# Kernel tuning notes

Hardware: AMD Instinct MI355X
Metric: run time of the kernel (lower is better)

## Reference

```python
import jax, jax.numpy as jnp
import numpy as np

B, S, T = 32, 512, 128   # batch, source chars, target (protoform) chars
V, L = 128, 5            # char vocab len(C2I), number of languages
E, H, F = 512, 1024, 2048  # embedding_dim, model_size, feedforward_dim
START_CHAR, SEP_LANG = 1, L - 1


def setup_inputs() -> dict:
    key = jax.random.key(0)
    ks = jax.random.split(key, 32)
    f32 = jnp.float32

    def n(k, shape, fan_in):
        return jax.random.normal(k, shape, dtype=f32) * (1.0 / np.sqrt(fan_in))

    inp = {
        "src_chars": jax.random.randint(ks[0], (B, S), 0, V),
        "src_langs": jax.random.randint(ks[1], (B, S), 0, L),
        "tgt_chars": jax.random.randint(ks[2], (B, T), 0, V),
        # embedding feature extractor
        "char_emb": jax.random.normal(ks[3], (V, E), dtype=f32) * 0.02,
        "lang_emb": jax.random.normal(ks[4], (L, E), dtype=f32) * 0.02,
        "fc_W": n(ks[5], (E, 2 * E), 2 * E),
        "fc_b": jnp.zeros((E,), f32),
        # encoder GRU (PyTorch gate layout r,z,n)
        "enc_Wi": n(ks[6], (3 * H, E), E),
        "enc_Wh": n(ks[7], (3 * H, H), H),
        "enc_bi": jnp.zeros((3 * H,), f32),
        "enc_bh": jnp.zeros((3 * H,), f32),
        # decoder GRU, input = [E ; H]
        "dec_Wi": n(ks[8], (3 * H, E + H), E + H),
        "dec_Wh": n(ks[9], (3 * H, H), H),
        "dec_bi": jnp.zeros((3 * H,), f32),
        "dec_bh": jnp.zeros((3 * H,), f32),
        # attention
        "Wq": n(ks[10], (H, H), H),
        "Wk": n(ks[11], (H, H), H),
        "Wcs": n(ks[12], (H, E), E),
        # MLP H -> 2F -> F -> V
        "W1": n(ks[13], (2 * F, H), H),
        "b1": jnp.zeros((2 * F,), f32),
        "W2": n(ks[14], (F, 2 * F), 2 * F),
        "b2": jnp.zeros((F,), f32),
        "W3": n(ks[15], (V, F), F),
    }
    return inp


def _gru_step(h, x, Wi, Wh, bi, bh):
    gi = x @ Wi.T + bi            # [B, 3H]
    gh = h @ Wh.T + bh            # [B, 3H]
    ir, iz, inn = jnp.split(gi, 3, axis=-1)
    hr, hz, hn = jnp.split(gh, 3, axis=-1)
    r = jax.nn.sigmoid(ir + hr)
    z = jax.nn.sigmoid(iz + hz)
    n = jnp.tanh(inn + r * hn)
    return (1.0 - z) * n + z * h


def _mlp(x, W1, b1, W2, b2, W3):
    h = jax.nn.relu(x @ W1.T + b1)
    h = jax.nn.relu(h @ W2.T + b2)
    return h @ W3.T               # [B, V]


def reference(src_chars, src_langs, tgt_chars,
              char_emb, lang_emb, fc_W, fc_b,
              enc_Wi, enc_Wh, enc_bi, enc_bh,
              dec_Wi, dec_Wh, dec_bi, dec_bh,
              Wq, Wk, Wcs,
              W1, b1, W2, b2, W3):
    # --- feature extraction: concat(char_emb, lang_emb) -> Linear(2E -> E) ---
    def embed(c_idx, l_idx):
        ce = char_emb[c_idx]                       # [..., E]
        le = lang_emb[l_idx]                       # [..., E]
        return jnp.concatenate([ce, le], -1) @ fc_W.T + fc_b

    encoded = embed(src_chars, src_langs)          # [B, S, E]

    # --- encoder GRU over source chars ---
    def enc_step(h, x_t):
        h = _gru_step(h, x_t, enc_Wi, enc_Wh, enc_bi, enc_bh)
        return h, h

    h0 = jnp.zeros((encoded.shape[0], enc_Wh.shape[1]), encoded.dtype)
    _, enc_states = jax.lax.scan(enc_step, h0, jnp.swapaxes(encoded, 0, 1))
    enc_states = jnp.swapaxes(enc_states, 0, 1)    # [B, S, H]

    # precompute attention values: W_c_s(encoded) + W_key(keys)  [B, S, H]
    att_vals = encoded @ Wcs.T + enc_states @ Wk.T

    # --- initial decoder step: <s> embedding + last encoder state ---
    start_emb = embed(jnp.full((encoded.shape[0],), START_CHAR),
                      jnp.full((encoded.shape[0],), SEP_LANG))  # [B, E]
    context0 = enc_states[:, -1]                   # [B, H]
    d0 = jnp.zeros_like(context0)
    dec_h = _gru_step(d0, jnp.concatenate([start_emb, context0], -1),
                      dec_Wi, dec_Wh, dec_bi, dec_bh)

    tgt_emb = embed(tgt_chars, jnp.full_like(tgt_chars, SEP_LANG))  # [B, T, E]

    # --- decode T steps with teacher forcing ---
    def dec_step(carry, x_t):
        h, ctx = carry
        scores_t = _mlp(h + ctx, W1, b1, W2, b2, W3)           # [B, V]
        q = h @ Wq.T                                           # [B, H]
        att = jnp.einsum('bsh,bh->bs', enc_states, q)
        w = jax.nn.softmax(att, axis=-1)
        ctx_new = jnp.einsum('bs,bsh->bh', w, att_vals)        # [B, H]
        h_new = _gru_step(h, jnp.concatenate([x_t, ctx_new], -1),
                          dec_Wi, dec_Wh, dec_bi, dec_bh)
        return (h_new, ctx_new), scores_t

    (_, _), scores = jax.lax.scan(dec_step, (dec_h, context0),
                                  jnp.swapaxes(tgt_emb, 0, 1))
    return jnp.swapaxes(scores, 0, 1)              # [B, T, V]
```

## Files before the change

### kernel.cpp

```cpp
#include <hip/hip_runtime.h>
#include <math.h>


#define Bb 32
#define Ss 512
#define Tt 128
#define Vv 128
#define Hh 1024
#define H3 3072
#define APAD 40

typedef __attribute__((ext_vector_type(8))) short bf16x8;
typedef __attribute__((ext_vector_type(4))) float f32x4;

__device__ inline f32x4 mfma_bf16(bf16x8 a, bf16x8 b, f32x4 c) {
  return __builtin_amdgcn_mfma_f32_16x16x32_bf16(a, b, c, 0, 0, 0);
}
__device__ inline unsigned short f2bf(float f) {
  unsigned u = __builtin_bit_cast(unsigned, f);
  unsigned r = (u + 0x7fffu + ((u >> 16) & 1u)) >> 16;
  return (unsigned short)r;
}
__device__ inline float lof(unsigned u) { return __builtin_bit_cast(float, u << 16); }
__device__ inline float hif(unsigned u) { return __builtin_bit_cast(float, u & 0xffff0000u); }
__device__ inline float bf2f(unsigned short h) {
  return __builtin_bit_cast(float, ((unsigned)h) << 16);
}

#define O_ESBF   0UL
#define O_ESQ    33554432UL
#define O_AVBF   67108864UL
#define O_HCBF   100663296UL
#define O_WHE    109051904UL
#define O_WHD    115343360UL
#define O_WIC    121634816UL
#define O_WKB    127926272UL
#define O_WQT    130023424UL
#define O_W1B    132120576UL
#define O_W2B    140509184UL
#define O_W3B    157286400UL
#define O_XCAT   157810688UL
#define O_EMBFC  160432128UL
#define O_GITAB  161742848UL
#define O_AVTAB  169607168UL
#define O_DGIXT  172228608UL
#define O_GH     173801472UL
#define O_GI     174194688UL
#define O_H      174587904UL
#define O_HBF    174718976UL
#define O_CTX    174784512UL
#define O_CTXBF  174915584UL
#define O_ATTL   174981120UL

__global__ void k_xcat(const float* __restrict__ ce, const float* __restrict__ le,
                       float* __restrict__ xcat) {
  int row = blockIdx.x;
  int l = row >> 7, c = row & 127;
  int i = threadIdx.x * 4;
  float4 v;
  if (i < 512) v = *(const float4*)(ce + c * 512 + i);
  else         v = *(const float4*)(le + l * 512 + (i - 512));
  *(float4*)(xcat + (size_t)row * 1024 + i) = v;
}

__global__ void k_cvt(const float* __restrict__ src, int ld, int lc,
                      unsigned short* __restrict__ dst) {
  size_t i = ((size_t)blockIdx.x * 256 + threadIdx.x) * 8;
  size_t r = i >> lc;
  int c = (int)(i & ((1u << lc) - 1));
  const float* s = src + r * (size_t)ld + c;
  float4 v0 = *(const float4*)s;
  float4 v1 = *(const float4*)(s + 4);
  union { unsigned short us[8]; uint4 u; } o;
  o.us[0] = f2bf(v0.x); o.us[1] = f2bf(v0.y); o.us[2] = f2bf(v0.z); o.us[3] = f2bf(v0.w);
  o.us[4] = f2bf(v1.x); o.us[5] = f2bf(v1.y); o.us[6] = f2bf(v1.z); o.us[7] = f2bf(v1.w);
  *(uint4*)(dst + i) = o.u;
}

__global__ void k_transcvt(const float* __restrict__ in, unsigned short* __restrict__ out) {
  __shared__ float t[32][33];
  int c0 = blockIdx.x * 32, r0 = blockIdx.y * 32;
  int tx = threadIdx.x, ty = threadIdx.y;
  for (int i = ty; i < 32; i += 8)
    t[i][tx] = in[(size_t)(r0 + i) * 1024 + c0 + tx];
  __syncthreads();
  for (int i = ty; i < 32; i += 8)
    out[(size_t)(c0 + i) * 1024 + r0 + tx] = f2bf(t[tx][i]);
}

template <bool BIAS>
__global__ __launch_bounds__(256) void k_gemm(
    const float* __restrict__ A, int lda, const float* __restrict__ W, int ldw,
    const float* __restrict__ bias, float* __restrict__ C, int ldc, int K) {
  __shared__ float As[8][128];
  __shared__ float Ws[8][128];
  int tid = threadIdx.x;
  int n0 = blockIdx.x * 128, m0 = blockIdx.y * 128;
  int tx = tid & 15, ty = tid >> 4;
  int lrow = tid >> 1, lseg = (tid & 1) * 4;
  const float* Ap = A + (size_t)(m0 + lrow) * lda + lseg;
  const float* Wp = W + (size_t)(n0 + lrow) * ldw + lseg;
  float acc[8][8];
#pragma unroll
  for (int i = 0; i < 8; ++i)
#pragma unroll
    for (int j = 0; j < 8; ++j) acc[i][j] = 0.f;
  for (int kt = 0; kt < K; kt += 8) {
    float4 av = *(const float4*)(Ap + kt);
    float4 wv = *(const float4*)(Wp + kt);
    __syncthreads();
    As[lseg + 0][lrow] = av.x; As[lseg + 1][lrow] = av.y;
    As[lseg + 2][lrow] = av.z; As[lseg + 3][lrow] = av.w;
    Ws[lseg + 0][lrow] = wv.x; Ws[lseg + 1][lrow] = wv.y;
    Ws[lseg + 2][lrow] = wv.z; Ws[lseg + 3][lrow] = wv.w;
    __syncthreads();
#pragma unroll
    for (int kk = 0; kk < 8; ++kk) {
      float a[8], b[8];
      *(float4*)(a + 0) = *(const float4*)(&As[kk][ty * 8 + 0]);
      *(float4*)(a + 4) = *(const float4*)(&As[kk][ty * 8 + 4]);
      *(float4*)(b + 0) = *(const float4*)(&Ws[kk][tx * 8 + 0]);
      *(float4*)(b + 4) = *(const float4*)(&Ws[kk][tx * 8 + 4]);
#pragma unroll
      for (int i = 0; i < 8; ++i)
#pragma unroll
        for (int j = 0; j < 8; ++j) acc[i][j] = fmaf(a[i], b[j], acc[i][j]);
    }
  }
#pragma unroll
  for (int i = 0; i < 8; ++i) {
    int r = m0 + ty * 8 + i;
#pragma unroll
    for (int j = 0; j < 8; ++j) {
      int c = n0 + tx * 8 + j;
      float v = acc[i][j];
      if (BIAS) v += bias[c];
      C[(size_t)r * ldc + c] = v;
    }
  }
}

template <int EPI, bool RELU, bool BIAS>
__global__ __launch_bounds__(256) void k_bgemm(
    const unsigned short* __restrict__ A, int lda,
    const unsigned short* __restrict__ W, int ldw,
    const float* __restrict__ bias, void* __restrict__ Cout, int ldc, int K,
    const float* __restrict__ avtab, const int* __restrict__ gl,
    const int* __restrict__ gc) {
  __shared__ unsigned short As[128 * APAD];
  __shared__ unsigned short Bs[128 * APAD];
  int tid = threadIdx.x;
  int n0 = blockIdx.x * 128, m0 = blockIdx.y * 128;
  int w = tid >> 6, l = tid & 63;
  int mw = (w & 1) * 64, nw = (w >> 1) * 64;
  int lrow = tid >> 1, lk = (tid & 1) * 16;
  const unsigned short* Ap = A + (size_t)(m0 + lrow) * lda + lk;
  const unsigned short* Wp = W + (size_t)(n0 + lrow) * ldw + lk;
  int fr = l & 15, fk = (l >> 4) * 8;
  f32x4 acc[4][4];
#pragma unroll
  for (int i = 0; i < 4; ++i)
#pragma unroll
    for (int j = 0; j < 4; ++j) acc[i][j] = (f32x4){0.f, 0.f, 0.f, 0.f};
  for (int kt = 0; kt < K; kt += 32) {
    uint4 a0 = *(const uint4*)(Ap + kt);
    uint4 a1 = *(const uint4*)(Ap + kt + 8);
    uint4 b0 = *(const uint4*)(Wp + kt);
    uint4 b1 = *(const uint4*)(Wp + kt + 8);
    __syncthreads();
    *(uint4*)&As[lrow * APAD + lk] = a0;
    *(uint4*)&As[lrow * APAD + lk + 8] = a1;
    *(uint4*)&Bs[lrow * APAD + lk] = b0;
    *(uint4*)&Bs[lrow * APAD + lk + 8] = b1;
    __syncthreads();
    bf16x8 af[4], bfg[4];
#pragma unroll
    for (int i = 0; i < 4; ++i) af[i] = *(const bf16x8*)&As[(mw + i * 16 + fr) * APAD + fk];
#pragma unroll
    for (int j = 0; j < 4; ++j) bfg[j] = *(const bf16x8*)&Bs[(nw + j * 16 + fr) * APAD + fk];
#pragma unroll
    for (int i = 0; i < 4; ++i)
#pragma unroll
      for (int j = 0; j < 4; ++j) acc[i][j] = mfma_bf16(af[i], bfg[j], acc[i][j]);
  }
#pragma unroll
  for (int i = 0; i < 4; ++i)
#pragma unroll
    for (int j = 0; j < 4; ++j) {
      int col = n0 + nw + j * 16 + fr;
#pragma unroll
      for (int r = 0; r < 4; ++r) {
        int row = m0 + mw + i * 16 + (l >> 4) * 4 + r;
        float v = acc[i][j][r];
        if (BIAS) v += bias[col];
        if (RELU) v = fmaxf(v, 0.f);
        if (EPI == 0) {
          ((unsigned short*)Cout)[(size_t)row * ldc + col] = f2bf(v);
        } else if (EPI == 1) {
          int cl = gl[row] * 128 + gc[row];
          ((unsigned short*)Cout)[(size_t)row * ldc + col] =
              f2bf(v + avtab[(size_t)cl * 1024 + col]);
        } else {
          int tt = row >> 5, bb = row & 31;
          ((float*)Cout)[(size_t)bb * (Tt * Vv) + tt * Vv + col] = v;
        }
      }
    }
}

__global__ __launch_bounds__(256) void k_rec(
    const unsigned short* __restrict__ A, const unsigned short* __restrict__ W,
    float* __restrict__ C, int N, int nrec,
    const unsigned short* __restrict__ esq, const float* __restrict__ h,
    const float* __restrict__ ctx, float* __restrict__ attL,
    unsigned short* __restrict__ hc) {
  __shared__ unsigned short As[32 * 1024];
  int tid = threadIdx.x;
  int id = blockIdx.x;
  if (id < nrec) {
    {
      const uint4* src = (const uint4*)A;
      uint4* dst = (uint4*)As;
#pragma unroll
      for (int i = 0; i < 16; ++i) {
        int c = i * 256 + tid;
        int m = c >> 7, kc = c & 127;
        dst[m * 128 + (kc ^ (m & 7))] = src[c];
      }
    }
    __syncthreads();
    int w = tid >> 6, l = tid & 63;
    int nb = id * 64 + w * 16;
    int fr = l & 15, fk8 = (l >> 4);
    const unsigned short* Wp = W + (size_t)(nb + fr) * 1024 + fk8 * 8;
    const bf16x8* Asv = (const bf16x8*)As;
    f32x4 acc0 = (f32x4){0.f, 0.f, 0.f, 0.f}, acc1 = acc0;
#pragma unroll 8
    for (int kt = 0; kt < 1024; kt += 32) {
      int kc8 = (kt >> 3) + fk8;
      bf16x8 bw = *(const bf16x8*)(Wp + kt);
      bf16x8 a0 = Asv[fr * 128 + (kc8 ^ (fr & 7))];
      bf16x8 a1 = Asv[(fr + 16) * 128 + (kc8 ^ (fr & 7))];
      acc0 = mfma_bf16(a0, bw, acc0);
      acc1 = mfma_bf16(a1, bw, acc1);
    }
    int col = nb + fr;
    int rb = (l >> 4) * 4;
#pragma unroll
    for (int r = 0; r < 4; ++r) {
      C[(size_t)(rb + r) * N + col] = acc0[r];
      C[(size_t)(rb + r + 16) * N + col] = acc1[r];
    }
  } else {
    float* hs = (float*)As;
    int a = id - nrec, b = a >> 3, sc = a & 7;
    for (int i = tid; i < 1024; i += 256) hs[i] = h[b * 1024 + i];
    __syncthreads();
    if (sc < 4) {
      int j = sc * 256 + tid;
      hc[b * 1024 + j] = f2bf(hs[j] + ctx[b * 1024 + j]);
    }
    int sg = tid >> 2, li = tid & 3;
    int s = sc * 64 + sg;
    const unsigned short* ep = esq + (size_t)(b * 512 + s) * 1024;
    float acc = 0.f;
#pragma unroll 4
    for (int i = 0; i < 32; ++i) {
      int k = (i * 4 + li) * 8;
      uint4 e = *(const uint4*)(ep + k);
      float4 h0 = *(const float4*)&hs[k];
      float4 h1 = *(const float4*)&hs[k + 4];
      acc += lof(e.x) * h0.x + hif(e.x) * h0.y + lof(e.y) * h0.z + hif(e.y) * h0.w +
             lof(e.z) * h1.x + hif(e.z) * h1.y + lof(e.w) * h1.z + hif(e.w) * h1.w;
    }
    acc += __shfl_xor(acc, 1);
    acc += __shfl_xor(acc, 2);
    if (li == 0) attL[b * 512 + s] = acc;
  }
}

__global__ void k_gates_enc(const float* __restrict__ gh, const float* __restrict__ gitab,
                            const int* __restrict__ sc, const int* __restrict__ sl,
                            const float* __restrict__ bh, float* __restrict__ h,
                            unsigned short* __restrict__ hbf, unsigned short* __restrict__ esb,
                            int s, int first) {
  int idx = blockIdx.x * 256 + threadIdx.x;
  int b = idx >> 10, j = idx & 1023;
  float ghr = bh[j], ghz = bh[1024 + j], ghn = bh[2048 + j];
  if (!first) {
    const float* g = gh + b * H3 + j;
    ghr += g[0]; ghz += g[1024]; ghn += g[2048];
  }
  int cl = sl[b * Ss + s] * 128 + sc[b * Ss + s];
  const float* gi = gitab + (size_t)cl * H3 + j;
  float r = 1.f / (1.f + expf(-(gi[0] + ghr)));
  float z = 1.f / (1.f + expf(-(gi[1024] + ghz)));
  float n = tanhf(gi[2048] + r * ghn);
  float hold = first ? 0.f : h[idx];
  float hn = (1.f - z) * n + z * hold;
  h[idx] = hn;
  unsigned short hb = f2bf(hn);
  hbf[idx] = hb;
  esb[(size_t)(b * Ss + s) * Hh + j] = hb;
}

__global__ void k_gates_dec(const float* __restrict__ gi, const float* __restrict__ gh,
                            const float* __restrict__ dgixt, const int* __restrict__ tgt,
                            const float* __restrict__ bh, float* __restrict__ h,
                            unsigned short* __restrict__ hbf, int t, int hzero, int usestart) {
  int idx = blockIdx.x * 256 + threadIdx.x;
  int b = idx >> 10, j = idx & 1023;
  const float* gp = gi + b * H3 + j;
  float gir = gp[0], giz = gp[1024], gin = gp[2048];
  float ghr = bh[j], ghz = bh[1024 + j], ghn = bh[2048 + j];
  if (!hzero) {
    const float* g = gh + b * H3 + j;
    ghr += g[0]; ghz += g[1024]; ghn += g[2048];
  }
  int c = usestart ? 1 : tgt[b * Tt + t];
  const float* gx = dgixt + (size_t)c * H3 + j;
  gir += gx[0]; giz += gx[1024]; gin += gx[2048];
  float r = 1.f / (1.f + expf(-(gir + ghr)));
  float z = 1.f / (1.f + expf(-(giz + ghz)));
  float n = tanhf(gin + r * ghn);
  float hold = hzero ? 0.f : h[idx];
  float hn = (1.f - z) * n + z * hold;
  h[idx] = hn;
  hbf[idx] = f2bf(hn);
}

__global__ void k_ctxinit(const float* __restrict__ h, float* __restrict__ ctx,
                          unsigned short* __restrict__ ctxbf) {
  int idx = blockIdx.x * 256 + threadIdx.x;
  float v = h[idx];
  ctx[idx] = v;
  ctxbf[idx] = f2bf(v);
}

__global__ __launch_bounds__(256) void k_ctxsm(const float* __restrict__ attL,
                                               const unsigned short* __restrict__ av,
                                               float* __restrict__ ctx,
                                               unsigned short* __restrict__ ctxbf) {
  int jt = blockIdx.x, b = blockIdx.y;
  __shared__ float w[512];
  __shared__ float wm[4];
  __shared__ float wsm[4];
  __shared__ float red2[128];
  int tid = threadIdx.x;
  float a0 = attL[b * Ss + tid * 2];
  float a1 = attL[b * Ss + tid * 2 + 1];
  float m = fmaxf(a0, a1);
  for (int d = 1; d < 64; d <<= 1) m = fmaxf(m, __shfl_xor(m, d));
  if ((tid & 63) == 0) wm[tid >> 6] = m;
  __syncthreads();
  m = fmaxf(fmaxf(wm[0], wm[1]), fmaxf(wm[2], wm[3]));
  float e0 = expf(a0 - m), e1 = expf(a1 - m);
  w[tid * 2] = e0;
  w[tid * 2 + 1] = e1;
  float ssum = e0 + e1;
  for (int d = 1; d < 64; d <<= 1) ssum += __shfl_xor(ssum, d);
  if ((tid & 63) == 0) wsm[tid >> 6] = ssum;
  __syncthreads();
  float scale = 1.f / (wsm[0] + wsm[1] + wsm[2] + wsm[3]);
  int j = jt * 128 + (tid & 127);
  int sh = tid >> 7;
  const unsigned short* avp = av + (size_t)(b * Ss + sh * 256) * Hh + j;
  float acc = 0.f;
#pragma unroll 16
  for (int s = 0; s < 256; ++s) acc += w[sh * 256 + s] * bf2f(avp[(size_t)s * Hh]);
  if (sh == 1) red2[tid & 127] = acc;
  __syncthreads();
  if (sh == 0) {
    float v = (acc + red2[tid & 127]) * scale;
    ctx[b * Hh + j] = v;
    ctxbf[b * Hh + j] = f2bf(v);
  }
}

extern "C" void kernel_launch(void* const* d_in, const int* in_sizes, int n_in,
                              void* d_out, int out_size, void* d_ws, size_t ws_size,
                              hipStream_t stream) {
  (void)in_sizes; (void)n_in; (void)out_size; (void)ws_size;
  const int*   src_chars = (const int*)d_in[0];
  const int*   src_langs = (const int*)d_in[1];
  const int*   tgt_chars = (const int*)d_in[2];
  const float* char_emb  = (const float*)d_in[3];
  const float* lang_emb  = (const float*)d_in[4];
  const float* fc_W  = (const float*)d_in[5];
  const float* fc_b  = (const float*)d_in[6];
  const float* enc_Wi = (const float*)d_in[7];
  const float* enc_Wh = (const float*)d_in[8];
  const float* enc_bi = (const float*)d_in[9];
  const float* enc_bh = (const float*)d_in[10];
  const float* dec_Wi = (const float*)d_in[11];
  const float* dec_Wh = (const float*)d_in[12];
  const float* dec_bi = (const float*)d_in[13];
  const float* dec_bh = (const float*)d_in[14];
  const float* Wq  = (const float*)d_in[15];
  const float* Wk  = (const float*)d_in[16];
  const float* Wcs = (const float*)d_in[17];
  const float* W1 = (const float*)d_in[18];
  const float* b1 = (const float*)d_in[19];
  const float* W2 = (const float*)d_in[20];
  const float* b2 = (const float*)d_in[21];
  const float* W3 = (const float*)d_in[22];
  float* out = (float*)d_out;

  char* ws = (char*)d_ws;
  unsigned short* esbf  = (unsigned short*)(ws + O_ESBF);
  unsigned short* esq   = (unsigned short*)(ws + O_ESQ);
  unsigned short* avbf  = (unsigned short*)(ws + O_AVBF);
  unsigned short* hcbf  = (unsigned short*)(ws + O_HCBF);
  unsigned short* WheB  = (unsigned short*)(ws + O_WHE);
  unsigned short* WhdB  = (unsigned short*)(ws + O_WHD);
  unsigned short* WicB  = (unsigned short*)(ws + O_WIC);
  unsigned short* WkB   = (unsigned short*)(ws + O_WKB);
  unsigned short* WqTB  = (unsigned short*)(ws + O_WQT);
  unsigned short* W1B   = (unsigned short*)(ws + O_W1B);
  unsigned short* W2B   = (unsigned short*)(ws + O_W2B);
  unsigned short* W3B   = (unsigned short*)(ws + O_W3B);
  float* xcat   = (float*)(ws + O_XCAT);
  float* embfc  = (float*)(ws + O_EMBFC);
  float* gitab  = (float*)(ws + O_GITAB);
  float* avtab  = (float*)(ws + O_AVTAB);
  float* dgixt  = (float*)(ws + O_DGIXT);
  float* ghbuf  = (float*)(ws + O_GH);
  float* gibuf  = (float*)(ws + O_GI);
  float* h      = (float*)(ws + O_H);
  unsigned short* hbf   = (unsigned short*)(ws + O_HBF);
  float* ctx    = (float*)(ws + O_CTX);
  unsigned short* ctxbf = (unsigned short*)(ws + O_CTXBF);
  float* attL   = (float*)(ws + O_ATTL);
  unsigned short* G1 = esq;
  unsigned short* G2 = avbf;

  dim3 blk(256);

  k_xcat<<<640, blk, 0, stream>>>(char_emb, lang_emb, xcat);
  k_gemm<true><<<dim3(4, 5), blk, 0, stream>>>(xcat, 1024, fc_W, 1024, fc_b, embfc, 512, 1024);
  k_gemm<true><<<dim3(24, 5), blk, 0, stream>>>(embfc, 512, enc_Wi, 512, enc_bi, gitab, H3, 512);
  k_gemm<false><<<dim3(8, 5), blk, 0, stream>>>(embfc, 512, Wcs, 512, nullptr, avtab, Hh, 512);
  k_gemm<true><<<dim3(24, 1), blk, 0, stream>>>(embfc + 512 * 512, 512, dec_Wi, 1536, dec_bi,
                                                dgixt, H3, 512);
  k_cvt<<<1536, blk, 0, stream>>>(enc_Wh, 1024, 10, WheB);
  k_cvt<<<1536, blk, 0, stream>>>(dec_Wh, 1024, 10, WhdB);
  k_cvt<<<1536, blk, 0, stream>>>(dec_Wi + 512, 1536, 10, WicB);
  k_cvt<<<512,  blk, 0, stream>>>(Wk, 1024, 10, WkB);
  k_cvt<<<2048, blk, 0, stream>>>(W1, 1024, 10, W1B);
  k_cvt<<<4096, blk, 0, stream>>>(W2, 4096, 12, W2B);
  k_cvt<<<128,  blk, 0, stream>>>(W3, 2048, 11, W3B);
  k_transcvt<<<dim3(32, 32), dim3(32, 8), 0, stream>>>(Wq, WqTB);

  for (int s = 0; s < Ss; ++s) {
    if (s > 0)
      k_rec<<<48, blk, 0, stream>>>(hbf, WheB, ghbuf, H3, 48,
                                    nullptr, nullptr, nullptr, nullptr, nullptr);
    k_gates_enc<<<128, blk, 0, stream>>>(ghbuf, gitab, src_chars, src_langs, enc_bh,
                                         h, hbf, esbf, s, s == 0 ? 1 : 0);
  }

  k_bgemm<0, false, false><<<dim3(8, 128), blk, 0, stream>>>(
      esbf, 1024, WqTB, 1024, nullptr, esq, 1024, 1024, nullptr, nullptr, nullptr);
  k_bgemm<1, false, false><<<dim3(8, 128), blk, 0, stream>>>(
      esbf, 1024, WkB, 1024, nullptr, avbf, 1024, 1024, avtab, src_langs, src_chars);

  k_ctxinit<<<128, blk, 0, stream>>>(h, ctx, ctxbf);
  k_rec<<<48, blk, 0, stream>>>(ctxbf, WicB, gibuf, H3, 48,
                                nullptr, nullptr, nullptr, nullptr, nullptr);
  k_gates_dec<<<128, blk, 0, stream>>>(gibuf, ghbuf, dgixt, tgt_chars, dec_bh,
                                       h, hbf, 0, 1, 1);

  for (int t = 0; t < Tt; ++t) {
    k_rec<<<304, blk, 0, stream>>>(hbf, WhdB, ghbuf, H3, 48,
                                   esq, h, ctx, attL, hcbf + (size_t)t * Bb * Hh);
    if (t == Tt - 1) break;
    k_ctxsm<<<dim3(8, 32), blk, 0, stream>>>(attL, avbf, ctx, ctxbf);
    k_rec<<<48, blk, 0, stream>>>(ctxbf, WicB, gibuf, H3, 48,
                                  nullptr, nullptr, nullptr, nullptr, nullptr);
    k_gates_dec<<<128, blk, 0, stream>>>(gibuf, ghbuf, dgixt, tgt_chars, dec_bh,
                                         h, hbf, t, 0, 0);
  }

  k_bgemm<0, true, true><<<dim3(32, 32), blk, 0, stream>>>(
      hcbf, 1024, W1B, 1024, b1, G1, 4096, 1024, nullptr, nullptr, nullptr);
  k_bgemm<0, true, true><<<dim3(16, 32), blk, 0, stream>>>(
      G1, 4096, W2B, 4096, b2, G2, 2048, 4096, nullptr, nullptr, nullptr);
  k_bgemm<2, false, false><<<dim3(1, 32), blk, 0, stream>>>(
      G2, 2048, W3B, 2048, nullptr, out, 0, 2048, nullptr, nullptr, nullptr);
}
```

Before: 9.582 ms.

## Fuse encoder GRU loop into one persistent kernel with grid barrier

Replaces the 512-step encoder loop, which launched a recurrent GEMM kernel and a gate kernel each step, with a single persistent kernel of 64 workgroups. Each workgroup owns 16 hidden units, computes its slice of h·Wh with MFMA, applies the gates in place, and synchronises with the others through an atomic counter barrier in global memory. The input-gate table is written in an interleaved r/z/n layout so each unit's three gate values sit next to each other. This is meant to remove roughly a thousand kernel launches and the round trips of intermediate gate buffers. In exchange it relies on all 64 workgroups being co-resident and on a spin-wait grid barrier every step.

```diff
diff --git a/kernel.cpp b/kernel.cpp
--- a/kernel.cpp
+++ b/kernel.cpp
@@ -9,6 +9,7 @@
 #define Hh 1024
 #define H3 3072
 #define APAD 40
+#define NWG 64
 
 typedef __attribute__((ext_vector_type(8))) short bf16x8;
 typedef __attribute__((ext_vector_type(4))) float f32x4;
@@ -51,6 +52,8 @@
 #define O_CTX    174784512UL
 #define O_CTXBF  174915584UL
 #define O_ATTL   174981120UL
+#define O_HB1    175046656UL
+#define O_BAR    175112192UL
 
 __global__ void k_xcat(const float* __restrict__ ce, const float* __restrict__ le,
                        float* __restrict__ xcat) {
@@ -88,7 +91,9 @@
     out[(size_t)(c0 + i) * 1024 + r0 + tx] = f2bf(t[tx][i]);
 }
 
-template <bool BIAS>
+__global__ void k_zerobar(unsigned* __restrict__ bar) { bar[threadIdx.x] = 0u; }
+
+template <bool BIAS, bool P3 = false>
 __global__ __launch_bounds__(256) void k_gemm(
     const float* __restrict__ A, int lda, const float* __restrict__ W, int ldw,
     const float* __restrict__ bias, float* __restrict__ C, int ldc, int K) {
@@ -135,8 +140,112 @@
       int c = n0 + tx * 8 + j;
       float v = acc[i][j];
       if (BIAS) v += bias[c];
-      C[(size_t)r * ldc + c] = v;
-    }
+      if (P3) C[((size_t)r * 1024 + (c & 1023)) * 3 + (c >> 10)] = v;
+      else    C[(size_t)r * ldc + c] = v;
+    }
+  }
+}
+
+__global__ __launch_bounds__(256) void k_enc(
+    const unsigned short* __restrict__ Whe, const float* __restrict__ gitabP,
+    const int* __restrict__ sc, const int* __restrict__ sl,
+    const float* __restrict__ bh,
+    unsigned short* __restrict__ hb0, unsigned short* __restrict__ hb1,
+    unsigned short* __restrict__ esb, float* __restrict__ hfinal,
+    unsigned* __restrict__ bar) {
+  __shared__ float red[4][48][33];
+  __shared__ float h_own[32][16];
+  int tid = threadIdx.x;
+  int g = blockIdx.x;
+  int w = tid >> 6, l = tid & 63;
+  int fr = l & 15, fk8 = l >> 4, rb = fk8 * 4;
+  int u = tid & 15, b0 = tid >> 4, b1 = b0 + 16;
+  int gu = g * 16 + u;
+  float bhr = bh[gu], bhz = bh[1024 + gu], bhn = bh[2048 + gu];
+  h_own[b0][u] = 0.f;
+  h_own[b1][u] = 0.f;
+  const unsigned short* Wp0 = Whe + (size_t)(g * 16 + fr) * 1024 + w * 256 + fk8 * 8;
+  const unsigned short* Wp1 = Wp0 + (size_t)1024 * 1024;
+  const unsigned short* Wp2 = Wp0 + (size_t)2048 * 1024;
+  for (int s = 0; s < Ss; ++s) {
+    const unsigned short* hbc = (s & 1) ? hb1 : hb0;
+    unsigned short* hbn = (s & 1) ? hb0 : hb1;
+    if (s > 0) {
+      const unsigned short* Ap = hbc + (size_t)fr * 1024 + w * 256 + fk8 * 8;
+      f32x4 acc[2][3];
+#pragma unroll
+      for (int i = 0; i < 2; ++i)
+#pragma unroll
+        for (int j = 0; j < 3; ++j) acc[i][j] = (f32x4){0.f, 0.f, 0.f, 0.f};
+#pragma unroll
+      for (int kt = 0; kt < 256; kt += 32) {
+        bf16x8 a0 = *(const bf16x8*)(Ap + kt);
+        bf16x8 a1 = *(const bf16x8*)(Ap + 16 * 1024 + kt);
+        bf16x8 w0 = *(const bf16x8*)(Wp0 + kt);
+        bf16x8 w1 = *(const bf16x8*)(Wp1 + kt);
+        bf16x8 w2 = *(const bf16x8*)(Wp2 + kt);
+        acc[0][0] = mfma_bf16(a0, w0, acc[0][0]);
+        acc[1][0] = mfma_bf16(a1, w0, acc[1][0]);
+        acc[0][1] = mfma_bf16(a0, w1, acc[0][1]);
+        acc[1][1] = mfma_bf16(a1, w1, acc[1][1]);
+        acc[0][2] = mfma_bf16(a0, w2, acc[0][2]);
+        acc[1][2] = mfma_bf16(a1, w2, acc[1][2]);
+      }
+#pragma unroll
+      for (int nt = 0; nt < 3; ++nt)
+#pragma unroll
+        for (int mt = 0; mt < 2; ++mt)
+#pragma unroll
+          for (int r = 0; r < 4; ++r)
+            red[w][nt * 16 + fr][mt * 16 + rb + r] = acc[mt][nt][r];
+    }
+    __syncthreads();
+    {
+      int cl0 = sl[b0 * Ss + s] * 128 + sc[b0 * Ss + s];
+      int cl1 = sl[b1 * Ss + s] * 128 + sc[b1 * Ss + s];
+      const float* gp0 = gitabP + ((size_t)cl0 * 1024 + gu) * 3;
+      const float* gp1 = gitabP + ((size_t)cl1 * 1024 + gu) * 3;
+      float gir0 = gp0[0], giz0 = gp0[1], gin0 = gp0[2];
+      float gir1 = gp1[0], giz1 = gp1[1], gin1 = gp1[2];
+      float ghr0 = bhr, ghz0 = bhz, ghn0 = bhn;
+      float ghr1 = bhr, ghz1 = bhz, ghn1 = bhn;
+      if (s > 0) {
+#pragma unroll
+        for (int ww = 0; ww < 4; ++ww) {
+          ghr0 += red[ww][u][b0]; ghz0 += red[ww][16 + u][b0]; ghn0 += red[ww][32 + u][b0];
+          ghr1 += red[ww][u][b1]; ghz1 += red[ww][16 + u][b1]; ghn1 += red[ww][32 + u][b1];
+        }
+      }
+      float r0 = 1.f / (1.f + expf(-(gir0 + ghr0)));
+      float z0 = 1.f / (1.f + expf(-(giz0 + ghz0)));
+      float n0 = tanhf(gin0 + r0 * ghn0);
+      float hv0 = (1.f - z0) * n0 + z0 * h_own[b0][u];
+      float r1 = 1.f / (1.f + expf(-(gir1 + ghr1)));
+      float z1 = 1.f / (1.f + expf(-(giz1 + ghz1)));
+      float n1 = tanhf(gin1 + r1 * ghn1);
+      float hv1 = (1.f - z1) * n1 + z1 * h_own[b1][u];
+      h_own[b0][u] = hv0;
+      h_own[b1][u] = hv1;
+      unsigned short q0 = f2bf(hv0), q1 = f2bf(hv1);
+      hbn[b0 * 1024 + gu] = q0;
+      hbn[b1 * 1024 + gu] = q1;
+      esb[((size_t)b0 * Ss + s) * 1024 + gu] = q0;
+      esb[((size_t)b1 * Ss + s) * 1024 + gu] = q1;
+      if (s == Ss - 1) {
+        hfinal[b0 * 1024 + gu] = hv0;
+        hfinal[b1 * 1024 + gu] = hv1;
+      }
+    }
+    __syncthreads();
+    if (tid == 0) {
+      __threadfence();
+      __hip_atomic_fetch_add(bar, 1u, __ATOMIC_RELEASE, __HIP_MEMORY_SCOPE_AGENT);
+      unsigned tgt = (unsigned)(s + 1) * NWG;
+      while (__hip_atomic_load(bar, __ATOMIC_ACQUIRE, __HIP_MEMORY_SCOPE_AGENT) < tgt)
+        __builtin_amdgcn_s_sleep(2);
+      __threadfence();
+    }
+    __syncthreads();
   }
 }
 
@@ -277,31 +386,6 @@
     acc += __shfl_xor(acc, 2);
     if (li == 0) attL[b * 512 + s] = acc;
   }
-}
-
-__global__ void k_gates_enc(const float* __restrict__ gh, const float* __restrict__ gitab,
-                            const int* __restrict__ sc, const int* __restrict__ sl,
-                            const float* __restrict__ bh, float* __restrict__ h,
-                            unsigned short* __restrict__ hbf, unsigned short* __restrict__ esb,
-                            int s, int first) {
-  int idx = blockIdx.x * 256 + threadIdx.x;
-  int b = idx >> 10, j = idx & 1023;
-  float ghr = bh[j], ghz = bh[1024 + j], ghn = bh[2048 + j];
-  if (!first) {
-    const float* g = gh + b * H3 + j;
-    ghr += g[0]; ghz += g[1024]; ghn += g[2048];
-  }
-  int cl = sl[b * Ss + s] * 128 + sc[b * Ss + s];
-  const float* gi = gitab + (size_t)cl * H3 + j;
-  float r = 1.f / (1.f + expf(-(gi[0] + ghr)));
-  float z = 1.f / (1.f + expf(-(gi[1024] + ghz)));
-  float n = tanhf(gi[2048] + r * ghn);
-  float hold = first ? 0.f : h[idx];
-  float hn = (1.f - z) * n + z * hold;
-  h[idx] = hn;
-  unsigned short hb = f2bf(hn);
-  hbf[idx] = hb;
-  esb[(size_t)(b * Ss + s) * Hh + j] = hb;
 }
 
 __global__ void k_gates_dec(const float* __restrict__ gi, const float* __restrict__ gh,
@@ -431,6 +515,8 @@
   float* ctx    = (float*)(ws + O_CTX);
   unsigned short* ctxbf = (unsigned short*)(ws + O_CTXBF);
   float* attL   = (float*)(ws + O_ATTL);
+  unsigned short* hbf2  = (unsigned short*)(ws + O_HB1);
+  unsigned*       bar   = (unsigned*)(ws + O_BAR);
   unsigned short* G1 = esq;
   unsigned short* G2 = avbf;
 
@@ -438,7 +524,8 @@
 
   k_xcat<<<640, blk, 0, stream>>>(char_emb, lang_emb, xcat);
   k_gemm<true><<<dim3(4, 5), blk, 0, stream>>>(xcat, 1024, fc_W, 1024, fc_b, embfc, 512, 1024);
-  k_gemm<true><<<dim3(24, 5), blk, 0, stream>>>(embfc, 512, enc_Wi, 512, enc_bi, gitab, H3, 512);
+  k_gemm<true, true><<<dim3(24, 5), blk, 0, stream>>>(embfc, 512, enc_Wi, 512, enc_bi,
+                                                      gitab, H3, 512);
   k_gemm<false><<<dim3(8, 5), blk, 0, stream>>>(embfc, 512, Wcs, 512, nullptr, avtab, Hh, 512);
   k_gemm<true><<<dim3(24, 1), blk, 0, stream>>>(embfc + 512 * 512, 512, dec_Wi, 1536, dec_bi,
                                                 dgixt, H3, 512);
@@ -451,13 +538,9 @@
   k_cvt<<<128,  blk, 0, stream>>>(W3, 2048, 11, W3B);
   k_transcvt<<<dim3(32, 32), dim3(32, 8), 0, stream>>>(Wq, WqTB);
 
-  for (int s = 0; s < Ss; ++s) {
-    if (s > 0)
-      k_rec<<<48, blk, 0, stream>>>(hbf, WheB, ghbuf, H3, 48,
-                                    nullptr, nullptr, nullptr, nullptr, nullptr);
-    k_gates_enc<<<128, blk, 0, stream>>>(ghbuf, gitab, src_chars, src_langs, enc_bh,
-                                         h, hbf, esbf, s, s == 0 ? 1 : 0);
-  }
+  k_zerobar<<<1, 64, 0, stream>>>(bar);
+  k_enc<<<NWG, blk, 0, stream>>>(WheB, gitab, src_chars, src_langs, enc_bh,
+                                 hbf, hbf2, esbf, h, bar);
 
   k_bgemm<0, false, false><<<dim3(8, 128), blk, 0, stream>>>(
       esbf, 1024, WqTB, 1024, nullptr, esq, 1024, 1024, nullptr, nullptr, nullptr);
```

After: 10.48 ms. 9.4% more time.

## Fuse GRU recurrent matvec with gate update per unit group, ping-pong hidden state

Applied to the files above, without the earlier changes.

Recurrent weights are repacked so each of 32 blocks owns 32 hidden units across all three gates. Each block computes the h@Wh (and ctx@Wic for the decoder) MFMA products, reduces them across K-split waves in shared memory, and applies the GRU gates in the same kernel. This removes the separate gates kernel and the gh/gi global round trip on every step. Input-gate tables are stored gate-interleaved, and bf16 hidden state is double-buffered to avoid a read/write race. The trade-off is only 32 blocks per step, and each wave reads A straight from global memory.

```diff
diff --git a/kernel.cpp b/kernel.cpp
--- a/kernel.cpp
+++ b/kernel.cpp
@@ -44,13 +44,12 @@
 #define O_GITAB  161742848UL
 #define O_AVTAB  169607168UL
 #define O_DGIXT  172228608UL
-#define O_GH     173801472UL
-#define O_GI     174194688UL
 #define O_H      174587904UL
 #define O_HBF    174718976UL
 #define O_CTX    174784512UL
 #define O_CTXBF  174915584UL
 #define O_ATTL   174981120UL
+#define O_HB1    175046656UL
 
 __global__ void k_xcat(const float* __restrict__ ce, const float* __restrict__ le,
                        float* __restrict__ xcat) {
@@ -88,7 +87,20 @@
     out[(size_t)(c0 + i) * 1024 + r0 + tx] = f2bf(t[tx][i]);
 }
 
-template <bool BIAS>
+__global__ void k_packw(const float* __restrict__ src, int ld,
+                        unsigned short* __restrict__ dst) {
+  int n = blockIdx.x;
+  int gate = n >> 10, unit = n & 1023;
+  int g = unit >> 5, ul = unit & 31;
+  size_t drow = (size_t)g * 96 + gate * 32 + ul;
+  int k = threadIdx.x * 4;
+  float4 v = *(const float4*)(src + (size_t)n * ld + k);
+  union { unsigned short us[4]; uint2 u; } o;
+  o.us[0] = f2bf(v.x); o.us[1] = f2bf(v.y); o.us[2] = f2bf(v.z); o.us[3] = f2bf(v.w);
+  *(uint2*)(dst + drow * 1024 + k) = o.u;
+}
+
+template <bool BIAS, bool P3 = false>
 __global__ __launch_bounds__(256) void k_gemm(
     const float* __restrict__ A, int lda, const float* __restrict__ W, int ldw,
     const float* __restrict__ bias, float* __restrict__ C, int ldc, int K) {
@@ -135,9 +147,174 @@
       int c = n0 + tx * 8 + j;
       float v = acc[i][j];
       if (BIAS) v += bias[c];
-      C[(size_t)r * ldc + c] = v;
-    }
-  }
+      if (P3) C[((size_t)r * 1024 + (c & 1023)) * 3 + (c >> 10)] = v;
+      else    C[(size_t)r * ldc + c] = v;
+    }
+  }
+}
+
+__global__ __launch_bounds__(256) void k_encstep(
+    const unsigned short* __restrict__ Wp, const float* __restrict__ gitabP,
+    const int* __restrict__ sc, const int* __restrict__ sl,
+    const float* __restrict__ bh, const unsigned short* __restrict__ hin,
+    unsigned short* __restrict__ hout, unsigned short* __restrict__ esb,
+    float* __restrict__ hf, int s, int first) {
+  __shared__ float red[4][96][36];
+  int tid = threadIdx.x, g = blockIdx.x;
+  int w = tid >> 6, l = tid & 63;
+  int fr = l & 15, fo = l >> 4;
+  if (!first) {
+    const unsigned short* Ab = hin + (size_t)fr * 1024 + w * 256 + fo * 8;
+    const unsigned short* Bp = Wp + ((size_t)g * 96 + fr) * 1024 + w * 256 + fo * 8;
+    f32x4 acc[2][6];
+#pragma unroll
+    for (int i = 0; i < 2; ++i)
+#pragma unroll
+      for (int j = 0; j < 6; ++j) acc[i][j] = (f32x4){0.f, 0.f, 0.f, 0.f};
+#pragma unroll
+    for (int ks = 0; ks < 8; ++ks) {
+      int ko = ks * 32;
+      bf16x8 a0 = *(const bf16x8*)(Ab + ko);
+      bf16x8 a1 = *(const bf16x8*)(Ab + 16 * 1024 + ko);
+#pragma unroll
+      for (int nt = 0; nt < 6; ++nt) {
+        bf16x8 bw = *(const bf16x8*)(Bp + (size_t)nt * 16 * 1024 + ko);
+        acc[0][nt] = mfma_bf16(a0, bw, acc[0][nt]);
+        acc[1][nt] = mfma_bf16(a1, bw, acc[1][nt]);
+      }
+    }
+#pragma unroll
+    for (int nt = 0; nt < 6; ++nt)
+#pragma unroll
+      for (int mt = 0; mt < 2; ++mt)
+        *(f32x4*)&red[w][nt * 16 + fr][mt * 16 + fo * 4] = acc[mt][nt];
+  }
+  __syncthreads();
+#pragma unroll
+  for (int i = 0; i < 4; ++i) {
+    int item = i * 256 + tid;
+    int ul = item & 31, b = item >> 5;
+    int gu = g * 32 + ul;
+    int cl = sl[b * Ss + s] * 128 + sc[b * Ss + s];
+    const float* gp = gitabP + ((size_t)cl * 1024 + gu) * 3;
+    float gir = gp[0], giz = gp[1], gin = gp[2];
+    float ghr = bh[gu], ghz = bh[1024 + gu], ghn = bh[2048 + gu];
+    if (!first) {
+#pragma unroll
+      for (int ww = 0; ww < 4; ++ww) {
+        ghr += red[ww][ul][b];
+        ghz += red[ww][32 + ul][b];
+        ghn += red[ww][64 + ul][b];
+      }
+    }
+    float r = 1.f / (1.f + expf(-(gir + ghr)));
+    float z = 1.f / (1.f + expf(-(giz + ghz)));
+    float n = tanhf(gin + r * ghn);
+    float hold = first ? 0.f : hf[b * 1024 + gu];
+    float hv = (1.f - z) * n + z * hold;
+    hf[b * 1024 + gu] = hv;
+    unsigned short q = f2bf(hv);
+    hout[b * 1024 + gu] = q;
+    esb[((size_t)b * Ss + s) * 1024 + gu] = q;
+  }
+}
+
+__global__ __launch_bounds__(256) void k_decstep(
+    const unsigned short* __restrict__ WicP, const unsigned short* __restrict__ WhdP,
+    const float* __restrict__ dgixtP, const int* __restrict__ tgt,
+    const float* __restrict__ bh, const unsigned short* __restrict__ ctxbf,
+    const unsigned short* __restrict__ hin, unsigned short* __restrict__ hout,
+    float* __restrict__ hf, int t, int first, int usestart) {
+  __shared__ float red[4][96][36];
+  int tid = threadIdx.x, g = blockIdx.x;
+  int w = tid >> 6, l = tid & 63;
+  int fr = l & 15, fo = l >> 4;
+  int gm = w >> 1, kb = (w & 1) * 512;
+  if (!(first && gm)) {
+    const unsigned short* A = gm ? hin : ctxbf;
+    const unsigned short* Wp = gm ? WhdP : WicP;
+    const unsigned short* Ab = A + (size_t)fr * 1024 + kb + fo * 8;
+    const unsigned short* Bp = Wp + ((size_t)g * 96 + fr) * 1024 + kb + fo * 8;
+    f32x4 acc[2][6];
+#pragma unroll
+    for (int i = 0; i < 2; ++i)
+#pragma unroll
+      for (int j = 0; j < 6; ++j) acc[i][j] = (f32x4){0.f, 0.f, 0.f, 0.f};
+#pragma unroll
+    for (int ks = 0; ks < 16; ++ks) {
+      int ko = ks * 32;
+      bf16x8 a0 = *(const bf16x8*)(Ab + ko);
+      bf16x8 a1 = *(const bf16x8*)(Ab + 16 * 1024 + ko);
+#pragma unroll
+      for (int nt = 0; nt < 6; ++nt) {
+        bf16x8 bw = *(const bf16x8*)(Bp + (size_t)nt * 16 * 1024 + ko);
+        acc[0][nt] = mfma_bf16(a0, bw, acc[0][nt]);
+        acc[1][nt] = mfma_bf16(a1, bw, acc[1][nt]);
+      }
+    }
+#pragma unroll
+    for (int nt = 0; nt < 6; ++nt)
+#pragma unroll
+      for (int mt = 0; mt < 2; ++mt)
+        *(f32x4*)&red[w][nt * 16 + fr][mt * 16 + fo * 4] = acc[mt][nt];
+  }
+  __syncthreads();
+#pragma unroll
+  for (int i = 0; i < 4; ++i) {
+    int item = i * 256 + tid;
+    int ul = item & 31, b = item >> 5;
+    int gu = g * 32 + ul;
+    int c = usestart ? 1 : tgt[b * Tt + t];
+    const float* gp = dgixtP + ((size_t)c * 1024 + gu) * 3;
+    float gir = gp[0] + red[0][ul][b] + red[1][ul][b];
+    float giz = gp[1] + red[0][32 + ul][b] + red[1][32 + ul][b];
+    float gin = gp[2] + red[0][64 + ul][b] + red[1][64 + ul][b];
+    float ghr = bh[gu], ghz = bh[1024 + gu], ghn = bh[2048 + gu];
+    if (!first) {
+      ghr += red[2][ul][b] + red[3][ul][b];
+      ghz += red[2][32 + ul][b] + red[3][32 + ul][b];
+      ghn += red[2][64 + ul][b] + red[3][64 + ul][b];
+    }
+    float r = 1.f / (1.f + expf(-(gir + ghr)));
+    float z = 1.f / (1.f + expf(-(giz + ghz)));
+    float n = tanhf(gin + r * ghn);
+    float hold = first ? 0.f : hf[b * 1024 + gu];
+    float hv = (1.f - z) * n + z * hold;
+    hf[b * 1024 + gu] = hv;
+    hout[b * 1024 + gu] = f2bf(hv);
+  }
+}
+
+__global__ __launch_bounds__(256) void k_att(const unsigned short* __restrict__ esq,
+                                             const float* __restrict__ h,
+                                             const float* __restrict__ ctx,
+                                             float* __restrict__ attL,
+                                             unsigned short* __restrict__ hc) {
+  __shared__ float hs[1024];
+  int tid = threadIdx.x;
+  int b = blockIdx.x >> 3, sc2 = blockIdx.x & 7;
+  for (int i = tid; i < 1024; i += 256) hs[i] = h[b * 1024 + i];
+  __syncthreads();
+  if (sc2 < 4) {
+    int j = sc2 * 256 + tid;
+    hc[b * 1024 + j] = f2bf(hs[j] + ctx[b * 1024 + j]);
+  }
+  int sg = tid >> 2, li = tid & 3;
+  int s = sc2 * 64 + sg;
+  const unsigned short* ep = esq + (size_t)(b * 512 + s) * 1024;
+  float acc = 0.f;
+#pragma unroll 4
+  for (int i = 0; i < 32; ++i) {
+    int k = (i * 4 + li) * 8;
+    uint4 e = *(const uint4*)(ep + k);
+    float4 h0 = *(const float4*)&hs[k];
+    float4 h1 = *(const float4*)&hs[k + 4];
+    acc += lof(e.x) * h0.x + hif(e.x) * h0.y + lof(e.y) * h0.z + hif(e.y) * h0.w +
+           lof(e.z) * h1.x + hif(e.z) * h1.y + lof(e.w) * h1.z + hif(e.w) * h1.w;
+  }
+  acc += __shfl_xor(acc, 1);
+  acc += __shfl_xor(acc, 2);
+  if (li == 0) attL[b * 512 + s] = acc;
 }
 
 template <int EPI, bool RELU, bool BIAS>
@@ -206,127 +383,6 @@
         }
       }
     }
-}
-
-__global__ __launch_bounds__(256) void k_rec(
-    const unsigned short* __restrict__ A, const unsigned short* __restrict__ W,
-    float* __restrict__ C, int N, int nrec,
-    const unsigned short* __restrict__ esq, const float* __restrict__ h,
-    const float* __restrict__ ctx, float* __restrict__ attL,
-    unsigned short* __restrict__ hc) {
-  __shared__ unsigned short As[32 * 1024];
-  int tid = threadIdx.x;
-  int id = blockIdx.x;
-  if (id < nrec) {
-    {
-      const uint4* src = (const uint4*)A;
-      uint4* dst = (uint4*)As;
-#pragma unroll
-      for (int i = 0; i < 16; ++i) {
-        int c = i * 256 + tid;
-        int m = c >> 7, kc = c & 127;
-        dst[m * 128 + (kc ^ (m & 7))] = src[c];
-      }
-    }
-    __syncthreads();
-    int w = tid >> 6, l = tid & 63;
-    int nb = id * 64 + w * 16;
-    int fr = l & 15, fk8 = (l >> 4);
-    const unsigned short* Wp = W + (size_t)(nb + fr) * 1024 + fk8 * 8;
-    const bf16x8* Asv = (const bf16x8*)As;
-    f32x4 acc0 = (f32x4){0.f, 0.f, 0.f, 0.f}, acc1 = acc0;
-#pragma unroll 8
-    for (int kt = 0; kt < 1024; kt += 32) {
-      int kc8 = (kt >> 3) + fk8;
-      bf16x8 bw = *(const bf16x8*)(Wp + kt);
-      bf16x8 a0 = Asv[fr * 128 + (kc8 ^ (fr & 7))];
-      bf16x8 a1 = Asv[(fr + 16) * 128 + (kc8 ^ (fr & 7))];
-      acc0 = mfma_bf16(a0, bw, acc0);
-      acc1 = mfma_bf16(a1, bw, acc1);
-    }
-    int col = nb + fr;
-    int rb = (l >> 4) * 4;
-#pragma unroll
-    for (int r = 0; r < 4; ++r) {
-      C[(size_t)(rb + r) * N + col] = acc0[r];
-      C[(size_t)(rb + r + 16) * N + col] = acc1[r];
-    }
-  } else {
-    float* hs = (float*)As;
-    int a = id - nrec, b = a >> 3, sc = a & 7;
-    for (int i = tid; i < 1024; i += 256) hs[i] = h[b * 1024 + i];
-    __syncthreads();
-    if (sc < 4) {
-      int j = sc * 256 + tid;
-      hc[b * 1024 + j] = f2bf(hs[j] + ctx[b * 1024 + j]);
-    }
-    int sg = tid >> 2, li = tid & 3;
-    int s = sc * 64 + sg;
-    const unsigned short* ep = esq + (size_t)(b * 512 + s) * 1024;
-    float acc = 0.f;
-#pragma unroll 4
-    for (int i = 0; i < 32; ++i) {
-      int k = (i * 4 + li) * 8;
-      uint4 e = *(const uint4*)(ep + k);
-      float4 h0 = *(const float4*)&hs[k];
-      float4 h1 = *(const float4*)&hs[k + 4];
-      acc += lof(e.x) * h0.x + hif(e.x) * h0.y + lof(e.y) * h0.z + hif(e.y) * h0.w +
-             lof(e.z) * h1.x + hif(e.z) * h1.y + lof(e.w) * h1.z + hif(e.w) * h1.w;
-    }
-    acc += __shfl_xor(acc, 1);
-    acc += __shfl_xor(acc, 2);
-    if (li == 0) attL[b * 512 + s] = acc;
-  }
-}
-
-__global__ void k_gates_enc(const float* __restrict__ gh, const float* __restrict__ gitab,
-                            const int* __restrict__ sc, const int* __restrict__ sl,
-                            const float* __restrict__ bh, float* __restrict__ h,
-                            unsigned short* __restrict__ hbf, unsigned short* __restrict__ esb,
-                            int s, int first) {
-  int idx = blockIdx.x * 256 + threadIdx.x;
-  int b = idx >> 10, j = idx & 1023;
-  float ghr = bh[j], ghz = bh[1024 + j], ghn = bh[2048 + j];
-  if (!first) {
-    const float* g = gh + b * H3 + j;
-    ghr += g[0]; ghz += g[1024]; ghn += g[2048];
-  }
-  int cl = sl[b * Ss + s] * 128 + sc[b * Ss + s];
-  const float* gi = gitab + (size_t)cl * H3 + j;
-  float r = 1.f / (1.f + expf(-(gi[0] + ghr)));
-  float z = 1.f / (1.f + expf(-(gi[1024] + ghz)));
-  float n = tanhf(gi[2048] + r * ghn);
-  float hold = first ? 0.f : h[idx];
-  float hn = (1.f - z) * n + z * hold;
-  h[idx] = hn;
-  unsigned short hb = f2bf(hn);
-  hbf[idx] = hb;
-  esb[(size_t)(b * Ss + s) * Hh + j] = hb;
-}
-
-__global__ void k_gates_dec(const float* __restrict__ gi, const float* __restrict__ gh,
-                            const float* __restrict__ dgixt, const int* __restrict__ tgt,
-                            const float* __restrict__ bh, float* __restrict__ h,
-                            unsigned short* __restrict__ hbf, int t, int hzero, int usestart) {
-  int idx = blockIdx.x * 256 + threadIdx.x;
-  int b = idx >> 10, j = idx & 1023;
-  const float* gp = gi + b * H3 + j;
-  float gir = gp[0], giz = gp[1024], gin = gp[2048];
-  float ghr = bh[j], ghz = bh[1024 + j], ghn = bh[2048 + j];
-  if (!hzero) {
-    const float* g = gh + b * H3 + j;
-    ghr += g[0]; ghz += g[1024]; ghn += g[2048];
-  }
-  int c = usestart ? 1 : tgt[b * Tt + t];
-  const float* gx = dgixt + (size_t)c * H3 + j;
-  gir += gx[0]; giz += gx[1024]; gin += gx[2048];
-  float r = 1.f / (1.f + expf(-(gir + ghr)));
-  float z = 1.f / (1.f + expf(-(giz + ghz)));
-  float n = tanhf(gin + r * ghn);
-  float hold = hzero ? 0.f : h[idx];
-  float hn = (1.f - z) * n + z * hold;
-  h[idx] = hn;
-  hbf[idx] = f2bf(hn);
 }
 
 __global__ void k_ctxinit(const float* __restrict__ h, float* __restrict__ ctx,
@@ -411,9 +467,9 @@
   unsigned short* esq   = (unsigned short*)(ws + O_ESQ);
   unsigned short* avbf  = (unsigned short*)(ws + O_AVBF);
   unsigned short* hcbf  = (unsigned short*)(ws + O_HCBF);
-  unsigned short* WheB  = (unsigned short*)(ws + O_WHE);
-  unsigned short* WhdB  = (unsigned short*)(ws + O_WHD);
-  unsigned short* WicB  = (unsigned short*)(ws + O_WIC);
+  unsigned short* WheP  = (unsigned short*)(ws + O_WHE);
+  unsigned short* WhdP  = (unsigned short*)(ws + O_WHD);
+  unsigned short* WicP  = (unsigned short*)(ws + O_WIC);
   unsigned short* WkB   = (unsigned short*)(ws + O_WKB);
   unsigned short* WqTB  = (unsigned short*)(ws + O_WQT);
   unsigned short* W1B   = (unsigned short*)(ws + O_W1B);
@@ -424,10 +480,9 @@
   float* gitab  = (float*)(ws + O_GITAB);
   float* avtab  = (float*)(ws + O_AVTAB);
   float* dgixt  = (float*)(ws + O_DGIXT);
-  float* ghbuf  = (float*)(ws + O_GH);
-  float* gibuf  = (float*)(ws + O_GI);
   float* h      = (float*)(ws + O_H);
-  unsigned short* hbf   = (unsigned short*)(ws + O_HBF);
+  unsigned short* he0   = (unsigned short*)(ws + O_HBF);
+  unsigned short* he1   = (unsigned short*)(ws + O_HB1);
   float* ctx    = (float*)(ws + O_CTX);
   unsigned short* ctxbf = (unsigned short*)(ws + O_CTXBF);
   float* attL   = (float*)(ws + O_ATTL);
@@ -438,13 +493,14 @@
 
   k_xcat<<<640, blk, 0, stream>>>(char_emb, lang_emb, xcat);
   k_gemm<true><<<dim3(4, 5), blk, 0, stream>>>(xcat, 1024, fc_W, 1024, fc_b, embfc, 512, 1024);
-  k_gemm<true><<<dim3(24, 5), blk, 0, stream>>>(embfc, 512, enc_Wi, 512, enc_bi, gitab, H3, 512);
+  k_gemm<true, true><<<dim3(24, 5), blk, 0, stream>>>(embfc, 512, enc_Wi, 512, enc_bi,
+                                                      gitab, H3, 512);
   k_gemm<false><<<dim3(8, 5), blk, 0, stream>>>(embfc, 512, Wcs, 512, nullptr, avtab, Hh, 512);
-  k_gemm<true><<<dim3(24, 1), blk, 0, stream>>>(embfc + 512 * 512, 512, dec_Wi, 1536, dec_bi,
-                                                dgixt, H3, 512);
-  k_cvt<<<1536, blk, 0, stream>>>(enc_Wh, 1024, 10, WheB);
-  k_cvt<<<1536, blk, 0, stream>>>(dec_Wh, 1024, 10, WhdB);
-  k_cvt<<<1536, blk, 0, stream>>>(dec_Wi + 512, 1536, 10, WicB);
+  k_gemm<true, true><<<dim3(24, 1), blk, 0, stream>>>(embfc + 512 * 512, 512, dec_Wi, 1536,
+                                                      dec_bi, dgixt, H3, 512);
+  k_packw<<<3072, blk, 0, stream>>>(enc_Wh, 1024, WheP);
+  k_packw<<<3072, blk, 0, stream>>>(dec_Wh, 1024, WhdP);
+  k_packw<<<3072, blk, 0, stream>>>(dec_Wi + 512, 1536, WicP);
   k_cvt<<<512,  blk, 0, stream>>>(Wk, 1024, 10, WkB);
   k_cvt<<<2048, blk, 0, stream>>>(W1, 1024, 10, W1B);
   k_cvt<<<4096, blk, 0, stream>>>(W2, 4096, 12, W2B);
@@ -452,11 +508,10 @@
   k_transcvt<<<dim3(32, 32), dim3(32, 8), 0, stream>>>(Wq, WqTB);
 
   for (int s = 0; s < Ss; ++s) {
-    if (s > 0)
-      k_rec<<<48, blk, 0, stream>>>(hbf, WheB, ghbuf, H3, 48,
-                                    nullptr, nullptr, nullptr, nullptr, nullptr);
-    k_gates_enc<<<128, blk, 0, stream>>>(ghbuf, gitab, src_chars, src_langs, enc_bh,
-                                         h, hbf, esbf, s, s == 0 ? 1 : 0);
+    const unsigned short* hin = (s & 1) ? he1 : he0;
+    unsigned short* hout = (s & 1) ? he0 : he1;
+    k_encstep<<<32, blk, 0, stream>>>(WheP, gitab, src_chars, src_langs, enc_bh,
+                                      hin, hout, esbf, h, s, s == 0 ? 1 : 0);
   }
 
   k_bgemm<0, false, false><<<dim3(8, 128), blk, 0, stream>>>(
@@ -465,20 +520,17 @@
       esbf, 1024, WkB, 1024, nullptr, avbf, 1024, 1024, avtab, src_langs, src_chars);
 
   k_ctxinit<<<128, blk, 0, stream>>>(h, ctx, ctxbf);
-  k_rec<<<48, blk, 0, stream>>>(ctxbf, WicB, gibuf, H3, 48,
-                                nullptr, nullptr, nullptr, nullptr, nullptr);
-  k_gates_dec<<<128, blk, 0, stream>>>(gibuf, ghbuf, dgixt, tgt_chars, dec_bh,
-                                       h, hbf, 0, 1, 1);
+  k_decstep<<<32, blk, 0, stream>>>(WicP, WhdP, dgixt, tgt_chars, dec_bh, ctxbf,
+                                    he1, he0, h, 0, 1, 1);
 
   for (int t = 0; t < Tt; ++t) {
-    k_rec<<<304, blk, 0, stream>>>(hbf, WhdB, ghbuf, H3, 48,
-                                   esq, h, ctx, attL, hcbf + (size_t)t * Bb * Hh);
+    k_att<<<256, blk, 0, stream>>>(esq, h, ctx, attL, hcbf + (size_t)t * Bb * Hh);
     if (t == Tt - 1) break;
     k_ctxsm<<<dim3(8, 32), blk, 0, stream>>>(attL, avbf, ctx, ctxbf);
-    k_rec<<<48, blk, 0, stream>>>(ctxbf, WicB, gibuf, H3, 48,
-                                  nullptr, nullptr, nullptr, nullptr, nullptr);
-    k_gates_dec<<<128, blk, 0, stream>>>(gibuf, ghbuf, dgixt, tgt_chars, dec_bh,
-                                         h, hbf, t, 0, 0);
+    const unsigned short* hin = (t & 1) ? he1 : he0;
+    unsigned short* hout = (t & 1) ? he0 : he1;
+    k_decstep<<<32, blk, 0, stream>>>(WicP, WhdP, dgixt, tgt_chars, dec_bh, ctxbf,
+                                      hin, hout, h, t, 0, 0);
   }
 
   k_bgemm<0, true, true><<<dim3(32, 32), blk, 0, stream>>>(
```

Result: slower. 12.63 ms (+31.8%).
